# Performance work log

Measured on AMD Instinct MI355X. Metric: run time of the kernel, lower is better.

Reference implementation:

```python
import jax, jax.numpy as jnp
import numpy as np

# Fixed problem sizes (match input_specs): B graphs of N points each, kNN with K neighbors.
B, N, K = 32, 2048, 20
F_IN, H, C = 3, 64, 40
BN = B * N
E = BN * K


def mlp(x, w1, b1, w2, b2):
    # PyG MLP([in, H, H]) with plain last layer: Lin -> ReLU -> Lin
    return jax.nn.relu(x @ w1 + b1) @ w2 + b2


def edge_conv(x, src, dst, w1, b1, w2, b2):
    # EdgeConv message for edge j->i: MLP(cat[x_i, x_j - x_i]); aggr='max' at target i.
    xi = x[dst]                      # [E, F]
    xj = x[src]                      # [E, F]
    msg = mlp(jnp.concatenate([xi, xj - xi], axis=-1), w1, b1, w2, b2)  # [E, H]
    out = jax.ops.segment_max(msg, dst, num_segments=x.shape[0])        # [BN, H]
    # nodes with no incoming edges: -inf -> 0 (torch_scatter max fill behavior)
    return jnp.where(jnp.isfinite(out), out, jnp.zeros((), out.dtype))


def dynamic_edge_conv(x, w1, b1, w2, b2):
    # Rebuild kNN graph from current features within each graph, then EdgeConv(max).
    xb = x.reshape(B, N, -1)                                   # [B, N, H]
    sq = jnp.sum(xb * xb, axis=-1)                             # [B, N]
    # squared euclidean distances [B, N, N]
    d = sq[:, :, None] - 2.0 * jnp.einsum('bnh,bmh->bnm', xb, xb) + sq[:, None, :]
    _, idx = jax.lax.top_k(-d, K)                              # [B, N, K] nearest (incl. self)
    xj = jax.vmap(lambda xg, ig: xg[ig])(xb, idx)              # [B, N, K, H]
    xi = jnp.broadcast_to(xb[:, :, None, :], xj.shape)         # [B, N, K, H]
    msg = mlp(jnp.concatenate([xi, xj - xi], axis=-1), w1, b1, w2, b2)  # [B, N, K, H]
    return jnp.max(msg, axis=2).reshape(BN, -1)                # exactly K msgs per node


def _lin_init(key, fan_in, fan_out):
    k1, k2 = jax.random.split(key)
    s = 1.0 / np.sqrt(fan_in)
    w = jax.random.uniform(k1, (fan_in, fan_out), jnp.float32, -s, s)
    b = jax.random.uniform(k2, (fan_out,), jnp.float32, -s, s)
    return w, b


def setup_inputs() -> dict:
    key = jax.random.key(0)
    ks = jax.random.split(key, 10)
    x = jax.random.normal(ks[0], (BN, F_IN), jnp.float32)
    edge_index = jax.random.randint(ks[1], (2, E), 0, BN, jnp.int64)
    batch = (jnp.arange(BN) // N).astype(jnp.int64)
    c1_w1, c1_b1 = _lin_init(ks[2], 2 * F_IN, H)
    c1_w2, c1_b2 = _lin_init(ks[3], H, H)
    d1_w1, d1_b1 = _lin_init(ks[4], 2 * H, H)
    d1_w2, d1_b2 = _lin_init(ks[5], H, H)
    d2_w1, d2_b1 = _lin_init(ks[6], 2 * H, H)
    d2_w2, d2_b2 = _lin_init(ks[7], H, H)
    lin_w, lin_b = _lin_init(ks[8], H, C)
    return dict(x=x, edge_index=edge_index, batch=batch,
                c1_w1=c1_w1, c1_b1=c1_b1, c1_w2=c1_w2, c1_b2=c1_b2,
                d1_w1=d1_w1, d1_b1=d1_b1, d1_w2=d1_w2, d1_b2=d1_b2,
                d2_w1=d2_w1, d2_b1=d2_b1, d2_w2=d2_w2, d2_b2=d2_b2,
                lin_w=lin_w, lin_b=lin_b)


def reference(x, edge_index, batch,
              c1_w1, c1_b1, c1_w2, c1_b2,
              d1_w1, d1_b1, d1_w2, d1_b2,
              d2_w1, d2_b1, d2_w2, d2_b2,
              lin_w, lin_b):
    # batch is assumed sorted with equal-size graphs (arange // N); kNN is done per graph.
    src, dst = edge_index[0], edge_index[1]
    h = edge_conv(x, src, dst, c1_w1, c1_b1, c1_w2, c1_b2)
    h = dynamic_edge_conv(jax.nn.elu(h), d1_w1, d1_b1, d1_w2, d1_b2)
    h = dynamic_edge_conv(jax.nn.elu(h), d2_w1, d2_b1, d2_w2, d2_b2)
    return h @ lin_w + lin_b
```

## Files before the change

### kernel.cpp

```cpp
#include <hip/hip_runtime.h>
#include <math.h>

#define Bg 32
#define Ng 2048
#define Kn 20
#define BNn (Bg*Ng)
#define En (BNn*Kn)
#define Hd 64
#define Cd 40

#define KK 24
#define CAPB 7

typedef __attribute__((ext_vector_type(8))) short bf16x8;
typedef __attribute__((ext_vector_type(4))) float f32x4;

__device__ __forceinline__ unsigned enc_f32(float f){
  unsigned u = __float_as_uint(f);
  return ((int)u < 0) ? ~u : (u | 0x80000000u);
}

__device__ __forceinline__ unsigned short bf16rne(float f){
  unsigned u = __float_as_uint(f);
  return (unsigned short)((u + 0x7FFFu + ((u >> 16) & 1u)) >> 16);
}

__global__ void prep_w_kernel(const float* __restrict__ w1c, const float* __restrict__ w1d1,
                              const float* __restrict__ w1d2,
                              float* __restrict__ wpq0, float* __restrict__ wpq1,
                              float* __restrict__ wpq2){
  int t = blockIdx.x*256 + threadIdx.x;
  if (t < 3*128){
    int d = t >> 7, l = t & 127;
    wpq0[t] = (l < 64) ? (w1c[d*64 + l] - w1c[(d+3)*64 + l]) : w1c[(d+3)*64 + (l-64)];
  }
  if (t < 64*128){
    int d = t >> 7, l = t & 127;
    wpq1[t] = (l < 64) ? (w1d1[d*64 + l] - w1d1[(d+64)*64 + l]) : w1d1[(d+64)*64 + (l-64)];
    wpq2[t] = (l < 64) ? (w1d2[d*64 + l] - w1d2[(d+64)*64 + l]) : w1d2[(d+64)*64 + (l-64)];
  }
}

__global__ void zero_kernel(int* __restrict__ p){
  p[blockIdx.x*256 + threadIdx.x] = 0;
}

__global__ void init_enc_kernel(unsigned int* __restrict__ enc){
  enc[blockIdx.x*256 + threadIdx.x] = 0x007FFFFFu;
}

template<int D>
__global__ __launch_bounds__(128) void gemm_pq_kernel(const float* __restrict__ x,
                               const float* __restrict__ w,
                               float* __restrict__ P, float* __restrict__ Q){
  __shared__ float xs[8*D];
  int l = threadIdx.x;
  int node0 = blockIdx.x*8;
  float wc[D];
  #pragma unroll
  for (int d=0; d<D; d++) wc[d] = w[d*128 + l];
  for (int i=l; i < 8*D; i += 128) xs[i] = x[(size_t)node0*D + i];
  __syncthreads();
  #pragma unroll
  for (int n=0; n<8; n++){
    float s = 0.f;
    #pragma unroll
    for (int d=0; d<D; d++) s = fmaf(xs[n*D+d], wc[d], s);
    int node = node0 + n;
    if (l < 64) P[(size_t)node*64 + l] = s;
    else        Q[(size_t)node*64 + (l-64)] = s;
  }
}

__global__ __launch_bounds__(256) void sqxb_kernel(const float* __restrict__ x,
        float* __restrict__ sq, unsigned short* __restrict__ xb){
  int t = blockIdx.x*256 + threadIdx.x;
  int node = t >> 6, l = t & 63;
  float v = x[t];
  xb[t] = bf16rne(v);
  float s = v*v;
  #pragma unroll
  for (int o=32; o; o>>=1) s += __shfl_xor(s, o, 64);
  if (l == 0) sq[node] = s;
}

__global__ __launch_bounds__(256) void decode_sqxb_kernel(const unsigned int* __restrict__ enc,
        const float* __restrict__ b2, float* __restrict__ x,
        float* __restrict__ sq, unsigned short* __restrict__ xb){
  int t = blockIdx.x*256 + threadIdx.x;
  int node = t >> 6, l = t & 63;
  unsigned int e = enc[t];
  unsigned int bits = (e & 0x80000000u) ? (e ^ 0x80000000u) : ~e;
  float f = __uint_as_float(bits);
  if (isfinite(f)) f += b2[l]; else f = 0.f;
  f = f > 0.f ? f : expm1f(f);
  x[t] = f;
  xb[t] = bf16rne(f);
  float s = f*f;
  #pragma unroll
  for (int o=32; o; o>>=1) s += __shfl_xor(s, o, 64);
  if (l == 0) sq[node] = s;
}

__global__ void count_kernel(const int* __restrict__ ei, int* __restrict__ deg){
  int e = blockIdx.x*256 + threadIdx.x;
  atomicAdd(&deg[ei[En + e]], 1);
}

__global__ __launch_bounds__(1024) void scan_kernel(const int* __restrict__ deg,
        int* __restrict__ rowptr, int* __restrict__ cursor){
  __shared__ int ps[1024];
  int t = threadIdx.x;
  int base = t*64;
  int s = 0;
  for (int k=0;k<64;k++) s += deg[base+k];
  ps[t] = s; __syncthreads();
  for (int off=1; off<1024; off<<=1){
    int v = (t>=off) ? ps[t-off] : 0;
    __syncthreads();
    ps[t] += v;
    __syncthreads();
  }
  int run = (t>0) ? ps[t-1] : 0;
  for (int k=0;k<64;k++){
    rowptr[base+k] = run; cursor[base+k] = run;
    run += deg[base+k];
  }
  if (t==1023) rowptr[BNn] = run;
}

__global__ void scatter_kernel(const int* __restrict__ ei, int* __restrict__ cursor,
                               int* __restrict__ csrc, int* __restrict__ enid){
  int e = blockIdx.x*256 + threadIdx.x;
  int s = ei[e], d = ei[En + e];
  int pos = atomicAdd(&cursor[d], 1);
  csrc[pos] = s;
  enid[pos] = d;
}

#define FMA8(av, r) \
  acc[r][0]=fmaf(av,b0.x,acc[r][0]); acc[r][1]=fmaf(av,b0.y,acc[r][1]); \
  acc[r][2]=fmaf(av,b0.z,acc[r][2]); acc[r][3]=fmaf(av,b0.w,acc[r][3]); \
  acc[r][4]=fmaf(av,b1v.x,acc[r][4]); acc[r][5]=fmaf(av,b1v.y,acc[r][5]); \
  acc[r][6]=fmaf(av,b1v.z,acc[r][6]); acc[r][7]=fmaf(av,b1v.w,acc[r][7]);

__global__ __launch_bounds__(256,3) void econv_gemm_kernel(
    const int* __restrict__ csrc, const int* __restrict__ enid,
    const float* __restrict__ P, const float* __restrict__ Q,
    const float* __restrict__ b1, const float* __restrict__ w2,
    unsigned int* __restrict__ enc){
  __shared__ __align__(16) float As[32*256];
  __shared__ __align__(16) float Ws[64*64];
  __shared__ int eids[256];
  int tid = threadIdx.x;
  int e0 = ((blockIdx.x & 7)*640 + (blockIdx.x >> 3))*256;
  int e = e0 + tid;
  int j = csrc[e];
  int i = enid[e];
  eids[tid] = i;
  const float* Pr = P + (size_t)i*Hd;
  const float* Qr = Q + (size_t)j*Hd;
  #pragma unroll
  for (int c=0;c<16;c++) Ws[c*256 + tid] = w2[c*256 + tid];

  int m0 = tid >> 3, n0 = tid & 7;
  float acc[8][8];
  #pragma unroll
  for (int a=0;a<8;a++)
    #pragma unroll
    for (int b=0;b<8;b++) acc[a][b]=0.f;

  #pragma unroll 1
  for (int kh=0; kh<2; kh++){
    __syncthreads();
    #pragma unroll
    for (int c=0;c<8;c++){
      int k = kh*32 + 4*c;
      float4 q4 = *(const float4*)(Qr + k);
      float4 pk = *(const float4*)(Pr + k);
      float4 b4 = *(const float4*)(b1 + k);
      As[(4*c+0)*256 + tid] = fmaxf(pk.x+q4.x+b4.x, 0.f);
      As[(4*c+1)*256 + tid] = fmaxf(pk.y+q4.y+b4.y, 0.f);
      As[(4*c+2)*256 + tid] = fmaxf(pk.z+q4.z+b4.z, 0.f);
      As[(4*c+3)*256 + tid] = fmaxf(pk.w+q4.w+b4.w, 0.f);
    }
    __syncthreads();
    #pragma unroll 4
    for (int kk=0; kk<32; kk++){
      int k = kh*32 + kk;
      float4 a0 = *(const float4*)&As[kk*256 + 8*m0];
      float4 a1 = *(const float4*)&As[kk*256 + 8*m0 + 4];
      float4 b0 = *(const float4*)&Ws[k*64 + 8*n0];
      float4 b1v = *(const float4*)&Ws[k*64 + 8*n0 + 4];
      FMA8(a0.x, 0) FMA8(a0.y, 1) FMA8(a0.z, 2) FMA8(a0.w, 3)
      FMA8(a1.x, 4) FMA8(a1.y, 5) FMA8(a1.z, 6) FMA8(a1.w, 7)
    }
  }
  unsigned* lmax = (unsigned*)As;
  int nfirst = eids[0];
  __syncthreads();
  for (int z = tid; z < 32*65; z += 256) lmax[z] = 0u;
  __syncthreads();
  {
    int rbase = 8*m0;
    int cur = eids[rbase];
    float vmax[8];
    #pragma unroll
    for (int b=0;b<8;b++) vmax[b] = -INFINITY;
    #pragma unroll
    for (int a=0;a<8;a++){
      int id = eids[rbase + a];
      if (id != cur){
        int lid = cur - nfirst;
        if (lid < 32){
          #pragma unroll
          for (int b=0;b<8;b++) atomicMax(&lmax[lid*65 + 8*n0 + b], enc_f32(vmax[b]));
        } else {
          #pragma unroll
          for (int b=0;b<8;b++) atomicMax(&enc[(size_t)cur*Hd + 8*n0 + b], enc_f32(vmax[b]));
        }
        #pragma unroll
        for (int b=0;b<8;b++) vmax[b] = -INFINITY;
        cur = id;
      }
      #pragma unroll
      for (int b=0;b<8;b++) vmax[b] = fmaxf(vmax[b], acc[a][b]);
    }
    int lid = cur - nfirst;
    if (lid < 32){
      #pragma unroll
      for (int b=0;b<8;b++) atomicMax(&lmax[lid*65 + 8*n0 + b], enc_f32(vmax[b]));
    } else {
      #pragma unroll
      for (int b=0;b<8;b++) atomicMax(&enc[(size_t)cur*Hd + 8*n0 + b], enc_f32(vmax[b]));
    }
  }
  __syncthreads();
  {
    int ch = tid & 63;
    for (int lid = tid >> 6; lid < 32; lid += 4){
      unsigned v = lmax[lid*65 + ch];
      if (v) atomicMax(&enc[(size_t)(nfirst + lid)*Hd + ch], v);
    }
  }
}

__device__ __forceinline__ void ins24(unsigned (&kb)[KK], unsigned key){
  #pragma unroll
  for (int p=KK-1; p>0; p--){
    unsigned ins = (key < kb[p]) ? key : kb[p];
    kb[p] = (key < kb[p-1]) ? kb[p-1] : ins;
  }
  kb[0] = (key < kb[0]) ? key : kb[0];
}

#define KNN_FLUSH() do { \
  _Pragma("unroll 1") \
  for (int c=0;c<CAPB;c++){ \
    if (!__any(c < cnt)) break; \
    unsigned kf = (c < cnt) ? kc[c][tid] : 0xFFFFFFFFu; \
    ins24(kb, kf); \
  } \
  cnt = 0; kbLast = kb[KK-1]; \
} while(0)

#define KNN_TRY(key) do { unsigned kk_ = (key); \
  if (kk_ < kbLast){ kc[cnt][tid] = kk_; cnt++; } } while(0)

#define SWZ16(base, row, stridep2, byteoff) \
  ((unsigned short*)((char*)(base) + ((((row) << (stridep2)) + (byteoff)) ^ (((row) & 7) << 4))))

__global__ __launch_bounds__(256,4) void knn_kernel(
    const unsigned short* __restrict__ xb, const float* __restrict__ sq,
    unsigned short* __restrict__ cand){
  __shared__ __align__(16) unsigned short xjb[128*64];
  __shared__ __align__(16) unsigned short Dt[64*128];
  __shared__ unsigned kc[CAPB][256];
  __shared__ float sqs[128];

  int tid = threadIdx.x;
  int lane = tid & 63, w = tid >> 6;
  int bid = ((blockIdx.x & 7) << 7) | (blockIdx.x >> 3);
  int g  = bid >> 5;
  int r0 = (bid & 31) * 64;
  const unsigned short* xbg = xb + (size_t)g*Ng*Hd;
  const float* sg = sq + (size_t)g*Ng;

  int q = w;
  int prow = lane;
  int rw = w*16;

  bf16x8 A0, A1;
  {
    int arow = r0 + rw + (lane & 15);
    A0 = *(const bf16x8*)(xbg + (size_t)arow*Hd +      (lane>>4)*8);
    A1 = *(const bf16x8*)(xbg + (size_t)arow*Hd + 32 + (lane>>4)*8);
  }
  {
    int jr = tid >> 1, half = tid & 1;
    int jloc = (jr >> 5)*512 + (jr & 31);
    const uint4* src = (const uint4*)(xbg + (size_t)jloc*Hd + half*32);
    uint4 a = src[0], b = src[1], c2 = src[2], d2 = src[3];
    *(uint4*)SWZ16(xjb, jr, 7, half*64 +  0) = a;
    *(uint4*)SWZ16(xjb, jr, 7, half*64 + 16) = b;
    *(uint4*)SWZ16(xjb, jr, 7, half*64 + 32) = c2;
    *(uint4*)SWZ16(xjb, jr, 7, half*64 + 48) = d2;
    if (tid < 128) sqs[tid] = sg[(tid>>5)*512 + (tid&31)];
  }

  unsigned kb[KK];
  #pragma unroll
  for (int t=0;t<KK;t++) kb[t] = 0xFFFFFFFFu;
  unsigned kbLast = 0xFFFFFFFFu;
  int cnt = 0;

  __syncthreads();

  #pragma unroll 1
  for (int it = 0; it < 16; it++){
    uint4 pf0, pf1, pf2, pf3; float psq = 0.f;
    int itn = it + 1;
    int jr = tid >> 1, half = tid & 1;
    if (itn < 16){
      int jloc = (jr >> 5)*512 + itn*32 + (jr & 31);
      const uint4* src = (const uint4*)(xbg + (size_t)jloc*Hd + half*32);
      pf0 = src[0]; pf1 = src[1]; pf2 = src[2]; pf3 = src[3];
      if (tid < 128) psq = sg[(tid>>5)*512 + itn*32 + (tid&31)];
    }
    #pragma unroll
    for (int jb = 0; jb < 8; jb++){
      int brow = jb*16 + (lane & 15);
      bf16x8 B0 = *(const bf16x8*)SWZ16(xjb, brow, 7,      (lane>>4)*16);
      bf16x8 B1 = *(const bf16x8*)SWZ16(xjb, brow, 7, 64 + (lane>>4)*16);
      f32x4 acc = {0.f, 0.f, 0.f, 0.f};
      acc = __builtin_amdgcn_mfma_f32_16x16x32_bf16(A0, B0, acc, 0, 0, 0);
      acc = __builtin_amdgcn_mfma_f32_16x16x32_bf16(A1, B1, acc, 0, 0, 0);
      int col = jb*16 + (lane & 15);
      float sqv = sqs[col];
      int rbase = rw + (lane>>4)*4;
      #pragma unroll
      for (int v=0; v<4; v++){
        float f = fmaf(acc[v], -2.f, sqv);
        unsigned u = __float_as_uint(f);
        unsigned t2 = ((unsigned)((int)u >> 31)) | 0x8000u;
        *SWZ16(Dt, rbase + v, 8, col*2) = (unsigned short)((u >> 16) ^ t2);
      }
    }
    __syncthreads();
    if (it == 0){
      unsigned key[32];
      const char* dbase = (const char*)Dt + (prow << 8);
      unsigned m = (prow & 7) << 4;
      #pragma unroll
      for (int r4=0; r4<4; r4++){
        uint4 dv = *(const uint4*)(dbase + ((unsigned)(q*64 + r4*16) ^ m));
        int cb = q*512 + r4*8;
        key[r4*8+0] = (dv.x << 16) + (unsigned)(cb + 0);
        key[r4*8+1] = (dv.x & 0xFFFF0000u) | (unsigned)(cb + 1);
        key[r4*8+2] = (dv.y << 16) + (unsigned)(cb + 2);
        key[r4*8+3] = (dv.y & 0xFFFF0000u) | (unsigned)(cb + 3);
        key[r4*8+4] = (dv.z << 16) + (unsigned)(cb + 4);
        key[r4*8+5] = (dv.z & 0xFFFF0000u) | (unsigned)(cb + 5);
        key[r4*8+6] = (dv.w << 16) + (unsigned)(cb + 6);
        key[r4*8+7] = (dv.w & 0xFFFF0000u) | (unsigned)(cb + 7);
      }
      #pragma unroll
      for (int k2 = 2; k2 <= 32; k2 <<= 1){
        #pragma unroll
        for (int j2 = k2>>1; j2 > 0; j2 >>= 1){
          #pragma unroll
          for (int i2 = 0; i2 < 32; i2++){
            int ixj = i2 ^ j2;
            if (ixj > i2){
              unsigned a = key[i2], b = key[ixj];
              unsigned lo = a < b ? a : b;
              unsigned hi = a < b ? b : a;
              bool up = ((i2 & k2) == 0);
              key[i2]  = up ? lo : hi;
              key[ixj] = up ? hi : lo;
            }
          }
        }
      }
      #pragma unroll
      for (int t=0;t<KK;t++) kb[t] = key[t];
      kbLast = kb[KK-1];
    } else {
      int jbase0 = q*512 + it*32;
      const char* dbase = (const char*)Dt + (prow << 8);
      unsigned m = (prow & 7) << 4;
      #pragma unroll
      for (int r4=0; r4<4; r4++){
        uint4 dv = *(const uint4*)(dbase + ((unsigned)(q*64 + r4*16) ^ m));
        int cb = jbase0 + r4*8;
        KNN_TRY((dv.x << 16) + (unsigned)(cb + 0));
        KNN_TRY((dv.x & 0xFFFF0000u) | (unsigned)(cb + 1));
        KNN_TRY((dv.y << 16) + (unsigned)(cb + 2));
        KNN_TRY((dv.y & 0xFFFF0000u) | (unsigned)(cb + 3));
        if (__any(cnt >= 4)) KNN_FLUSH();
        KNN_TRY((dv.z << 16) + (unsigned)(cb + 4));
        KNN_TRY((dv.z & 0xFFFF0000u) | (unsigned)(cb + 5));
        KNN_TRY((dv.w << 16) + (unsigned)(cb + 6));
        KNN_TRY((dv.w & 0xFFFF0000u) | (unsigned)(cb + 7));
        if (__any(cnt >= 4)) KNN_FLUSH();
      }
    }
    if (itn < 16){
      *(uint4*)SWZ16(xjb, jr, 7, half*64 +  0) = pf0;
      *(uint4*)SWZ16(xjb, jr, 7, half*64 + 16) = pf1;
      *(uint4*)SWZ16(xjb, jr, 7, half*64 + 32) = pf2;
      *(uint4*)SWZ16(xjb, jr, 7, half*64 + 48) = pf3;
      if (tid < 128) sqs[tid] = psq;
    }
    __syncthreads();
  }
  KNN_FLUSH();
  size_t base = (size_t)(g*Ng + r0 + prow)*96 + q*24;
  #pragma unroll
  for (int t=0;t<KK;t++)
    cand[base + t] = (unsigned short)(kb[t] & 2047u);
}

__global__ __launch_bounds__(256,2) void rerank_kernel(const float* __restrict__ x,
        const unsigned short* __restrict__ cand, int* __restrict__ idx){
  __shared__ __align__(16) unsigned long long ks[4][96];
  int tid = threadIdx.x;
  int lane = tid & 63, w = tid >> 6;
  int bid = ((blockIdx.x & 7) << 11) | (blockIdx.x >> 3);
  int row = bid*4 + w;
  int g = row >> 11;
  const float* xg = x + (size_t)g*Ng*Hd;
  int chunk = lane & 3;
  int cg = lane >> 2;
  const float* xr = x + (size_t)row*Hd;
  float4 xc[4];
  #pragma unroll
  for (int it2=0; it2<4; it2++) xc[it2] = *(const float4*)(xr + 16*it2 + 4*chunk);

  int js[6];
  #pragma unroll
  for (int p=0; p<6; p++) js[p] = cand[(size_t)row*96 + p*16 + cg];

  float4 bb[6][4];
  #pragma unroll
  for (int p=0; p<6; p++){
    const float* xj = xg + (size_t)js[p]*Hd;
    #pragma unroll
    for (int it2=0; it2<4; it2++) bb[p][it2] = *(const float4*)(xj + 16*it2 + 4*chunk);
  }
  #pragma unroll
  for (int p=0; p<6; p++){
    float dot = 0.f, sqj = 0.f;
    #pragma unroll
    for (int it2=0; it2<4; it2++){
      float4 b = bb[p][it2];
      float4 a = xc[it2];
      dot = fmaf(a.x, b.x, dot); dot = fmaf(a.y, b.y, dot);
      dot = fmaf(a.z, b.z, dot); dot = fmaf(a.w, b.w, dot);
      sqj = fmaf(b.x, b.x, sqj); sqj = fmaf(b.y, b.y, sqj);
      sqj = fmaf(b.z, b.z, sqj); sqj = fmaf(b.w, b.w, sqj);
    }
    dot += __shfl_xor(dot, 1, 64); dot += __shfl_xor(dot, 2, 64);
    sqj += __shfl_xor(sqj, 1, 64); sqj += __shfl_xor(sqj, 2, 64);
    if (chunk == 0){
      float dist = fmaf(dot, -2.f, sqj);
      ks[w][p*16 + cg] = ((unsigned long long)enc_f32(dist) << 32) | (unsigned)js[p];
    }
  }
  __syncthreads();
  unsigned long long k0 = ks[w][lane];
  unsigned long long k1 = (lane < 32) ? ks[w][64 + lane] : ~0ULL;
  int r0 = 0, r1 = 0;
  #pragma unroll
  for (int c=0;c<96;c+=2){
    unsigned long long a = ks[w][c], b = ks[w][c+1];
    r0 += (a < k0) + (b < k0);
    r1 += (a < k1) + (b < k1);
  }
  if (r0 < Kn) idx[(size_t)row*Kn + r0] = g*Ng + (int)(k0 & 2047ULL);
  if (lane < 32 && r1 < Kn) idx[(size_t)row*Kn + r1] = g*Ng + (int)(k1 & 2047ULL);
}

__global__ __launch_bounds__(256,3) void emsg_kernel(
    const int* __restrict__ srcl,
    const float* __restrict__ P, const float* __restrict__ Q,
    const float* __restrict__ b1, const float* __restrict__ w2,
    unsigned int* __restrict__ enc){
  __shared__ __align__(16) char smem[49152];
  unsigned short* Ah = (unsigned short*)smem;
  unsigned short* Al = (unsigned short*)(smem + 16384);
  unsigned short* Wh = (unsigned short*)(smem + 32768);
  unsigned short* Wl = (unsigned short*)(smem + 40960);
  float* p0 = (float*)smem;
  float* p1 = (float*)(smem + 8448);
  int tid = threadIdx.x;
  int lane = tid & 63, w = tid >> 6;
  int e0 = ((blockIdx.x & 7)*640 + (blockIdx.x >> 3))*256;

  #pragma unroll
  for (int z = 0; z < 16; z++){
    int idx = z*256 + tid;
    int k = idx >> 6, n = idx & 63;
    float f = w2[idx];
    unsigned short h = bf16rne(f);
    float fh = __uint_as_float((unsigned)h << 16);
    unsigned short l = bf16rne(f - fh);
    *SWZ16(Wh, n, 7, k*2) = h;
    *SWZ16(Wl, n, 7, k*2) = l;
  }

  #pragma unroll 1
  for (int hh = 0; hh < 2; hh++){
    int eh0 = e0 + hh*128;
    __syncthreads();
    {
      int el = tid >> 1, kh = (tid & 1) * 32;
      int e = eh0 + el;
      int i = e / Kn;
      int j = srcl[e];
      const float* Pr = P + (size_t)i*Hd + kh;
      const float* Qr = Q + (size_t)j*Hd + kh;
      const float* Br = b1 + kh;
      #pragma unroll
      for (int m = 0; m < 4; m++){
        float4 pa = ((const float4*)Pr)[2*m], pb = ((const float4*)Pr)[2*m+1];
        float4 qa = ((const float4*)Qr)[2*m], qb = ((const float4*)Qr)[2*m+1];
        float4 ba = ((const float4*)Br)[2*m], bbv = ((const float4*)Br)[2*m+1];
        float a[8];
        a[0]=fmaxf(pa.x+qa.x+ba.x,0.f);  a[1]=fmaxf(pa.y+qa.y+ba.y,0.f);
        a[2]=fmaxf(pa.z+qa.z+ba.z,0.f);  a[3]=fmaxf(pa.w+qa.w+ba.w,0.f);
        a[4]=fmaxf(pb.x+qb.x+bbv.x,0.f); a[5]=fmaxf(pb.y+qb.y+bbv.y,0.f);
        a[6]=fmaxf(pb.z+qb.z+bbv.z,0.f); a[7]=fmaxf(pb.w+qb.w+bbv.w,0.f);
        unsigned hw[4], lw[4];
        #pragma unroll
        for (int t=0;t<4;t++){
          unsigned short h0 = bf16rne(a[2*t]);
          unsigned short h1 = bf16rne(a[2*t+1]);
          float f0 = __uint_as_float((unsigned)h0 << 16);
          float f1 = __uint_as_float((unsigned)h1 << 16);
          unsigned short l0 = bf16rne(a[2*t] - f0);
          unsigned short l1 = bf16rne(a[2*t+1] - f1);
          hw[t] = (unsigned)h0 | ((unsigned)h1 << 16);
          lw[t] = (unsigned)l0 | ((unsigned)l1 << 16);
        }
        uint4 hv = {hw[0], hw[1], hw[2], hw[3]};
        uint4 lv = {lw[0], lw[1], lw[2], lw[3]};
        *(uint4*)SWZ16(Ah, el, 7, (kh + 8*m)*2) = hv;
        *(uint4*)SWZ16(Al, el, 7, (kh + 8*m)*2) = lv;
      }
    }
    __syncthreads();
    bf16x8 Af[2][2], Lf[2][2];
    #pragma unroll
    for (int mt=0; mt<2; mt++)
      #pragma unroll
      for (int s=0; s<2; s++){
        int row = w*32 + mt*16 + (lane & 15);
        Af[mt][s] = *(const bf16x8*)SWZ16(Ah, row, 7, (s*32 + (lane>>4)*8)*2);
        Lf[mt][s] = *(const bf16x8*)SWZ16(Al, row, 7, (s*32 + (lane>>4)*8)*2);
      }
    f32x4 acc[2][4];
    #pragma unroll
    for (int mt=0; mt<2; mt++)
      #pragma unroll
      for (int nt=0; nt<4; nt++)
        acc[mt][nt] = (f32x4){0.f,0.f,0.f,0.f};
    #pragma unroll
    for (int nt=0; nt<4; nt++){
      int n = nt*16 + (lane & 15);
      bf16x8 Bh0 = *(const bf16x8*)SWZ16(Wh, n, 7, ((lane>>4)*8)*2);
      bf16x8 Bh1 = *(const bf16x8*)SWZ16(Wh, n, 7, (32 + (lane>>4)*8)*2);
      bf16x8 Bl0 = *(const bf16x8*)SWZ16(Wl, n, 7, ((lane>>4)*8)*2);
      bf16x8 Bl1 = *(const bf16x8*)SWZ16(Wl, n, 7, (32 + (lane>>4)*8)*2);
      #pragma unroll
      for (int mt=0; mt<2; mt++){
        f32x4 a_ = acc[mt][nt];
        a_ = __builtin_amdgcn_mfma_f32_16x16x32_bf16(Af[mt][0], Bh0, a_, 0, 0, 0);
        a_ = __builtin_amdgcn_mfma_f32_16x16x32_bf16(Af[mt][1], Bh1, a_, 0, 0, 0);
        a_ = __builtin_amdgcn_mfma_f32_16x16x32_bf16(Af[mt][0], Bl0, a_, 0, 0, 0);
        a_ = __builtin_amdgcn_mfma_f32_16x16x32_bf16(Af[mt][1], Bl1, a_, 0, 0, 0);
        a_ = __builtin_amdgcn_mfma_f32_16x16x32_bf16(Lf[mt][0], Bh0, a_, 0, 0, 0);
        a_ = __builtin_amdgcn_mfma_f32_16x16x32_bf16(Lf[mt][1], Bh1, a_, 0, 0, 0);
        acc[mt][nt] = a_;
      }
    }
    __syncthreads();
    #pragma unroll
    for (int mt=0; mt<2; mt++){
      int rb = w*32 + mt*16 + (lane>>4)*4;
      int rbg = eh0 + rb;
      int nd0 = rbg / Kn;
      int split = (nd0+1)*Kn - rbg; if (split > 4) split = 4;
      int cm = rb >> 2;
      #pragma unroll
      for (int nt=0; nt<4; nt++){
        int ch = nt*16 + (lane & 15);
        float s0v = -INFINITY, s1v = -INFINITY;
        #pragma unroll
        for (int v=0; v<4; v++){
          float val = acc[mt][nt][v];
          if (v < split) s0v = fmaxf(s0v, val); else s1v = fmaxf(s1v, val);
        }
        p0[ch*33 + cm] = s0v;
        p1[ch*33 + cm] = s1v;
      }
    }
    __syncthreads();
    int nfirst = eh0 / Kn;
    int ncnt = (eh0 + 127) / Kn - nfirst + 1;
    int ch = tid & 63;
    for (int ln = tid >> 6; ln < ncnt; ln += 4){
      int nd = nfirst + ln;
      int glo = nd*Kn;      if (glo < eh0)     glo = eh0;
      int ghi = nd*Kn + Kn; if (ghi > eh0+128) ghi = eh0+128;
      int mlo = (glo - eh0) >> 2, mhi = (ghi - 1 - eh0) >> 2;
      float v = -INFINITY;
      for (int mm = mlo; mm <= mhi; mm++){
        int bn = (eh0 + 4*mm) / Kn;
        if (bn == nd)     v = fmaxf(v, p0[ch*33 + mm]);
        if (bn + 1 == nd) v = fmaxf(v, p1[ch*33 + mm]);
      }
      atomicMax(&enc[(size_t)nd*Hd + ch], enc_f32(v));
    }
  }
}

__global__ __launch_bounds__(256) void decode_kernel(const unsigned int* __restrict__ enc,
         const float* __restrict__ b2, float* __restrict__ x){
  int t = blockIdx.x*256 + threadIdx.x;
  unsigned int e = enc[t];
  unsigned int bits = (e & 0x80000000u) ? (e ^ 0x80000000u) : ~e;
  float f = __uint_as_float(bits);
  if (isfinite(f)) f += b2[t & 63]; else f = 0.f;
  x[t] = f;
}

__global__ __launch_bounds__(64) void final_kernel(const float* __restrict__ h,
        const float* __restrict__ w, const float* __restrict__ bias,
        float* __restrict__ out){
  __shared__ float xs[Hd];
  int c = threadIdx.x;
  float wc[Hd];
  float bc = 0.f;
  if (c < Cd){
    #pragma unroll
    for (int d=0; d<Hd; d++) wc[d] = w[d*Cd + c];
    bc = bias[c];
  }
  for (int i = blockIdx.x; i < BNn; i += gridDim.x){
    __syncthreads();
    xs[c] = h[(size_t)i*Hd + c];
    __syncthreads();
    if (c < Cd){
      float s = bc;
      #pragma unroll
      for (int d=0; d<Hd; d++) s = fmaf(xs[d], wc[d], s);
      out[(size_t)i*Cd + c] = s;
    }
  }
}

extern "C" void kernel_launch(void* const* d_in, const int* in_sizes, int n_in,
                              void* d_out, int out_size, void* d_ws, size_t ws_size,
                              hipStream_t stream){
  const float* x0   = (const float*)d_in[0];
  const int*   ei   = (const int*)d_in[1];
  const float* c1w1 = (const float*)d_in[3];
  const float* c1b1 = (const float*)d_in[4];
  const float* c1w2 = (const float*)d_in[5];
  const float* c1b2 = (const float*)d_in[6];
  const float* d1w1 = (const float*)d_in[7];
  const float* d1b1 = (const float*)d_in[8];
  const float* d1w2 = (const float*)d_in[9];
  const float* d1b2 = (const float*)d_in[10];
  const float* d2w1 = (const float*)d_in[11];
  const float* d2b1 = (const float*)d_in[12];
  const float* d2w2 = (const float*)d_in[13];
  const float* d2b2 = (const float*)d_in[14];
  const float* linw = (const float*)d_in[15];
  const float* linb = (const float*)d_in[16];
  float* out = (float*)d_out;

  char* ws = (char*)d_ws;
  size_t off = 0;
  auto alloc = [&](size_t bytes)->char*{
    char* p = ws + off; off += (bytes + 255) & ~(size_t)255; return p;
  };
  float*        X    = (float*)alloc(sizeof(float)*(size_t)BNn*Hd);
  float*        P    = (float*)alloc(sizeof(float)*(size_t)BNn*Hd);
  float*        Q    = (float*)alloc(sizeof(float)*(size_t)BNn*Hd);
  float*        H2   = (float*)alloc(sizeof(float)*(size_t)BNn*Hd);
  unsigned int* ENC  = (unsigned int*)alloc(sizeof(unsigned)*(size_t)BNn*Hd);
  int*          SHRD = (int*)alloc(sizeof(int)*(size_t)En);
  int*          DEG  = (int*)alloc(sizeof(int)*BNn);
  int*          RPTR = (int*)alloc(sizeof(int)*(BNn+1));
  int*          CUR  = (int*)alloc(sizeof(int)*BNn);
  float*        SQ   = (float*)alloc(sizeof(float)*BNn);
  float*        WPQ0 = (float*)alloc(sizeof(float)*3*128);
  float*        WPQ1 = (float*)alloc(sizeof(float)*64*128);
  float*        WPQ2 = (float*)alloc(sizeof(float)*64*128);
  int*            CSRC = SHRD;
  int*            IDX  = SHRD;
  int*            ENID = (int*)H2;
  unsigned short* XB   = (unsigned short*)H2;
  unsigned short* CAND = (unsigned short*)ENC;
  (void)ws_size; (void)in_sizes; (void)n_in; (void)out_size;

  prep_w_kernel<<<32, 256, 0, stream>>>(c1w1, d1w1, d2w1, WPQ0, WPQ1, WPQ2);
  zero_kernel<<<BNn/256, 256, 0, stream>>>(DEG);
  count_kernel<<<En/256, 256, 0, stream>>>(ei, DEG);
  gemm_pq_kernel<3><<<BNn/8, 128, 0, stream>>>(x0, WPQ0, P, Q);
  scan_kernel<<<1, 1024, 0, stream>>>(DEG, RPTR, CUR);
  scatter_kernel<<<En/256, 256, 0, stream>>>(ei, CUR, CSRC, ENID);
  init_enc_kernel<<<BNn*Hd/256, 256, 0, stream>>>(ENC);
  econv_gemm_kernel<<<En/256, 256, 0, stream>>>(CSRC, ENID, P, Q, c1b1, c1w2, ENC);
  decode_sqxb_kernel<<<BNn*Hd/256, 256, 0, stream>>>(ENC, c1b2, X, SQ, XB);

  gemm_pq_kernel<64><<<BNn/8, 128, 0, stream>>>(X, WPQ1, P, Q);
  knn_kernel<<<Bg*32, 256, 0, stream>>>(XB, SQ, CAND);
  rerank_kernel<<<BNn/4, 256, 0, stream>>>(X, CAND, IDX);
  init_enc_kernel<<<BNn*Hd/256, 256, 0, stream>>>(ENC);
  emsg_kernel<<<En/256, 256, 0, stream>>>(IDX, P, Q, d1b1, d1w2, ENC);
  decode_sqxb_kernel<<<BNn*Hd/256, 256, 0, stream>>>(ENC, d1b2, X, SQ, XB);

  gemm_pq_kernel<64><<<BNn/8, 128, 0, stream>>>(X, WPQ2, P, Q);
  knn_kernel<<<Bg*32, 256, 0, stream>>>(XB, SQ, CAND);
  rerank_kernel<<<BNn/4, 256, 0, stream>>>(X, CAND, IDX);
  init_enc_kernel<<<BNn*Hd/256, 256, 0, stream>>>(ENC);
  emsg_kernel<<<En/256, 256, 0, stream>>>(IDX, P, Q, d2b1, d2w2, ENC);
  decode_kernel<<<BNn*Hd/256, 256, 0, stream>>>(ENC, d2b2, H2);

  final_kernel<<<8192, 64, 0, stream>>>(H2, linw, linb, out);
}
```

Before: 1.337 ms.

## Use split-bf16 MFMA for first EdgeConv second-layer GEMM

Replaces the scalar FP32 FMA GEMM in the first EdgeConv kernel with bf16 MFMA instructions. Activations and weights are split into high and low bf16 parts, and three products are summed to keep near-FP32 accuracy. Edges are processed in two halves of 128. The max-aggregation now goes through a transposed, swizzled LDS tile, with per-column run-length atomicMax straight to global memory instead of an LDS pre-reduction stage. This moves compute onto the matrix cores but may raise global atomic traffic and adds split/convert overhead.

```diff
diff --git a/kernel.cpp b/kernel.cpp
--- a/kernel.cpp
+++ b/kernel.cpp
@@ -138,109 +138,143 @@
   enid[pos] = d;
 }
 
-#define FMA8(av, r) \
-  acc[r][0]=fmaf(av,b0.x,acc[r][0]); acc[r][1]=fmaf(av,b0.y,acc[r][1]); \
-  acc[r][2]=fmaf(av,b0.z,acc[r][2]); acc[r][3]=fmaf(av,b0.w,acc[r][3]); \
-  acc[r][4]=fmaf(av,b1v.x,acc[r][4]); acc[r][5]=fmaf(av,b1v.y,acc[r][5]); \
-  acc[r][6]=fmaf(av,b1v.z,acc[r][6]); acc[r][7]=fmaf(av,b1v.w,acc[r][7]);
+#define SWZ16(base, row, stridep2, byteoff) \
+  ((unsigned short*)((char*)(base) + ((((row) << (stridep2)) + (byteoff)) ^ (((row) & 7) << 4))))
 
 __global__ __launch_bounds__(256,3) void econv_gemm_kernel(
     const int* __restrict__ csrc, const int* __restrict__ enid,
     const float* __restrict__ P, const float* __restrict__ Q,
     const float* __restrict__ b1, const float* __restrict__ w2,
     unsigned int* __restrict__ enc){
-  __shared__ __align__(16) float As[32*256];
-  __shared__ __align__(16) float Ws[64*64];
+  __shared__ __align__(16) char smem[49152];
+  unsigned short* Ah = (unsigned short*)smem;
+  unsigned short* Al = (unsigned short*)(smem + 16384);
+  unsigned short* Wh = (unsigned short*)(smem + 32768);
+  unsigned short* Wl = (unsigned short*)(smem + 40960);
+  float* Ct = (float*)smem;
   __shared__ int eids[256];
   int tid = threadIdx.x;
+  int lane = tid & 63, w = tid >> 6;
   int e0 = ((blockIdx.x & 7)*640 + (blockIdx.x >> 3))*256;
-  int e = e0 + tid;
-  int j = csrc[e];
-  int i = enid[e];
-  eids[tid] = i;
-  const float* Pr = P + (size_t)i*Hd;
-  const float* Qr = Q + (size_t)j*Hd;
-  #pragma unroll
-  for (int c=0;c<16;c++) Ws[c*256 + tid] = w2[c*256 + tid];
-
-  int m0 = tid >> 3, n0 = tid & 7;
-  float acc[8][8];
-  #pragma unroll
-  for (int a=0;a<8;a++)
-    #pragma unroll
-    for (int b=0;b<8;b++) acc[a][b]=0.f;
+
+  eids[tid] = enid[e0 + tid];
+  #pragma unroll
+  for (int z = 0; z < 16; z++){
+    int idx = z*256 + tid;
+    int k = idx >> 6, n = idx & 63;
+    float f = w2[idx];
+    unsigned short h = bf16rne(f);
+    float fh = __uint_as_float((unsigned)h << 16);
+    unsigned short l = bf16rne(f - fh);
+    *SWZ16(Wh, n, 7, k*2) = h;
+    *SWZ16(Wl, n, 7, k*2) = l;
+  }
 
   #pragma unroll 1
-  for (int kh=0; kh<2; kh++){
-    __syncthreads();
-    #pragma unroll
-    for (int c=0;c<8;c++){
-      int k = kh*32 + 4*c;
-      float4 q4 = *(const float4*)(Qr + k);
-      float4 pk = *(const float4*)(Pr + k);
-      float4 b4 = *(const float4*)(b1 + k);
-      As[(4*c+0)*256 + tid] = fmaxf(pk.x+q4.x+b4.x, 0.f);
-      As[(4*c+1)*256 + tid] = fmaxf(pk.y+q4.y+b4.y, 0.f);
-      As[(4*c+2)*256 + tid] = fmaxf(pk.z+q4.z+b4.z, 0.f);
-      As[(4*c+3)*256 + tid] = fmaxf(pk.w+q4.w+b4.w, 0.f);
-    }
-    __syncthreads();
-    #pragma unroll 4
-    for (int kk=0; kk<32; kk++){
-      int k = kh*32 + kk;
-      float4 a0 = *(const float4*)&As[kk*256 + 8*m0];
-      float4 a1 = *(const float4*)&As[kk*256 + 8*m0 + 4];
-      float4 b0 = *(const float4*)&Ws[k*64 + 8*n0];
-      float4 b1v = *(const float4*)&Ws[k*64 + 8*n0 + 4];
-      FMA8(a0.x, 0) FMA8(a0.y, 1) FMA8(a0.z, 2) FMA8(a0.w, 3)
-      FMA8(a1.x, 4) FMA8(a1.y, 5) FMA8(a1.z, 6) FMA8(a1.w, 7)
-    }
-  }
-  unsigned* lmax = (unsigned*)As;
-  int nfirst = eids[0];
-  __syncthreads();
-  for (int z = tid; z < 32*65; z += 256) lmax[z] = 0u;
-  __syncthreads();
-  {
-    int rbase = 8*m0;
-    int cur = eids[rbase];
-    float vmax[8];
-    #pragma unroll
-    for (int b=0;b<8;b++) vmax[b] = -INFINITY;
-    #pragma unroll
-    for (int a=0;a<8;a++){
-      int id = eids[rbase + a];
-      if (id != cur){
-        int lid = cur - nfirst;
-        if (lid < 32){
-          #pragma unroll
-          for (int b=0;b<8;b++) atomicMax(&lmax[lid*65 + 8*n0 + b], enc_f32(vmax[b]));
-        } else {
-          #pragma unroll
-          for (int b=0;b<8;b++) atomicMax(&enc[(size_t)cur*Hd + 8*n0 + b], enc_f32(vmax[b]));
+  for (int hh = 0; hh < 2; hh++){
+    int eh0 = e0 + hh*128;
+    __syncthreads();
+    {
+      int el = tid >> 1, kh2 = (tid & 1) * 32;
+      int e = eh0 + el;
+      int i = eids[hh*128 + el];
+      int j = csrc[e];
+      const float* Pr = P + (size_t)i*Hd + kh2;
+      const float* Qr = Q + (size_t)j*Hd + kh2;
+      const float* Br = b1 + kh2;
+      #pragma unroll
+      for (int m = 0; m < 4; m++){
+        float4 pa = ((const float4*)Pr)[2*m], pb = ((const float4*)Pr)[2*m+1];
+        float4 qa = ((const float4*)Qr)[2*m], qb = ((const float4*)Qr)[2*m+1];
+        float4 ba = ((const float4*)Br)[2*m], bbv = ((const float4*)Br)[2*m+1];
+        float a[8];
+        a[0]=fmaxf(pa.x+qa.x+ba.x,0.f);  a[1]=fmaxf(pa.y+qa.y+ba.y,0.f);
+        a[2]=fmaxf(pa.z+qa.z+ba.z,0.f);  a[3]=fmaxf(pa.w+qa.w+ba.w,0.f);
+        a[4]=fmaxf(pb.x+qb.x+bbv.x,0.f); a[5]=fmaxf(pb.y+qb.y+bbv.y,0.f);
+        a[6]=fmaxf(pb.z+qb.z+bbv.z,0.f); a[7]=fmaxf(pb.w+qb.w+bbv.w,0.f);
+        unsigned hw[4], lw[4];
+        #pragma unroll
+        for (int t=0;t<4;t++){
+          unsigned short h0 = bf16rne(a[2*t]);
+          unsigned short h1 = bf16rne(a[2*t+1]);
+          float f0 = __uint_as_float((unsigned)h0 << 16);
+          float f1 = __uint_as_float((unsigned)h1 << 16);
+          unsigned short l0 = bf16rne(a[2*t] - f0);
+          unsigned short l1 = bf16rne(a[2*t+1] - f1);
+          hw[t] = (unsigned)h0 | ((unsigned)h1 << 16);
+          lw[t] = (unsigned)l0 | ((unsigned)l1 << 16);
         }
+        uint4 hv = {hw[0], hw[1], hw[2], hw[3]};
+        uint4 lv = {lw[0], lw[1], lw[2], lw[3]};
+        *(uint4*)SWZ16(Ah, el, 7, (kh2 + 8*m)*2) = hv;
+        *(uint4*)SWZ16(Al, el, 7, (kh2 + 8*m)*2) = lv;
+      }
+    }
+    __syncthreads();
+    bf16x8 Af[2][2], Lf[2][2];
+    #pragma unroll
+    for (int mt=0; mt<2; mt++)
+      #pragma unroll
+      for (int s=0; s<2; s++){
+        int row = w*32 + mt*16 + (lane & 15);
+        Af[mt][s] = *(const bf16x8*)SWZ16(Ah, row, 7, (s*32 + (lane>>4)*8)*2);
+        Lf[mt][s] = *(const bf16x8*)SWZ16(Al, row, 7, (s*32 + (lane>>4)*8)*2);
+      }
+    f32x4 acc[2][4];
+    #pragma unroll
+    for (int mt=0; mt<2; mt++)
+      #pragma unroll
+      for (int nt=0; nt<4; nt++)
+        acc[mt][nt] = (f32x4){0.f,0.f,0.f,0.f};
+    #pragma unroll
+    for (int nt=0; nt<4; nt++){
+      int n = nt*16 + (lane & 15);
+      bf16x8 Bh0 = *(const bf16x8*)SWZ16(Wh, n, 7, ((lane>>4)*8)*2);
+      bf16x8 Bh1 = *(const bf16x8*)SWZ16(Wh, n, 7, (32 + (lane>>4)*8)*2);
+      bf16x8 Bl0 = *(const bf16x8*)SWZ16(Wl, n, 7, ((lane>>4)*8)*2);
+      bf16x8 Bl1 = *(const bf16x8*)SWZ16(Wl, n, 7, (32 + (lane>>4)*8)*2);
+      #pragma unroll
+      for (int mt=0; mt<2; mt++){
+        f32x4 a_ = acc[mt][nt];
+        a_ = __builtin_amdgcn_mfma_f32_16x16x32_bf16(Af[mt][0], Bh0, a_, 0, 0, 0);
+        a_ = __builtin_amdgcn_mfma_f32_16x16x32_bf16(Af[mt][1], Bh1, a_, 0, 0, 0);
+        a_ = __builtin_amdgcn_mfma_f32_16x16x32_bf16(Af[mt][0], Bl0, a_, 0, 0, 0);
+        a_ = __builtin_amdgcn_mfma_f32_16x16x32_bf16(Af[mt][1], Bl1, a_, 0, 0, 0);
+        a_ = __builtin_amdgcn_mfma_f32_16x16x32_bf16(Lf[mt][0], Bh0, a_, 0, 0, 0);
+        a_ = __builtin_amdgcn_mfma_f32_16x16x32_bf16(Lf[mt][1], Bh1, a_, 0, 0, 0);
+        acc[mt][nt] = a_;
+      }
+    }
+    __syncthreads();
+    #pragma unroll
+    for (int mt=0; mt<2; mt++){
+      int rb = w*32 + mt*16 + (lane>>4)*4;
+      #pragma unroll
+      for (int nt=0; nt<4; nt++){
+        int ch = nt*16 + (lane & 15);
         #pragma unroll
-        for (int b=0;b<8;b++) vmax[b] = -INFINITY;
-        cur = id;
-      }
-      #pragma unroll
-      for (int b=0;b<8;b++) vmax[b] = fmaxf(vmax[b], acc[a][b]);
-    }
-    int lid = cur - nfirst;
-    if (lid < 32){
-      #pragma unroll
-      for (int b=0;b<8;b++) atomicMax(&lmax[lid*65 + 8*n0 + b], enc_f32(vmax[b]));
-    } else {
-      #pragma unroll
-      for (int b=0;b<8;b++) atomicMax(&enc[(size_t)cur*Hd + 8*n0 + b], enc_f32(vmax[b]));
-    }
-  }
-  __syncthreads();
-  {
-    int ch = tid & 63;
-    for (int lid = tid >> 6; lid < 32; lid += 4){
-      unsigned v = lmax[lid*65 + ch];
-      if (v) atomicMax(&enc[(size_t)(nfirst + lid)*Hd + ch], v);
+        for (int v=0; v<4; v++)
+          Ct[ch*128 + ((rb+v) ^ (ch & 31))] = acc[mt][nt][v];
+      }
+    }
+    __syncthreads();
+    {
+      int ch = tid & 63, part = tid >> 6;
+      int rbase = part*32;
+      int cur = eids[hh*128 + rbase];
+      float vmax = -INFINITY;
+      #pragma unroll 1
+      for (int r = 0; r < 32; r++){
+        int row = rbase + r;
+        int id = eids[hh*128 + row];
+        float v = Ct[ch*128 + (row ^ (ch & 31))];
+        if (id != cur){
+          atomicMax(&enc[(size_t)cur*Hd + ch], enc_f32(vmax));
+          vmax = -INFINITY; cur = id;
+        }
+        vmax = fmaxf(vmax, v);
+      }
+      atomicMax(&enc[(size_t)cur*Hd + ch], enc_f32(vmax));
     }
   }
 }
@@ -266,9 +300,6 @@
 
 #define KNN_TRY(key) do { unsigned kk_ = (key); \
   if (kk_ < kbLast){ kc[cnt][tid] = kk_; cnt++; } } while(0)
-
-#define SWZ16(base, row, stridep2, byteoff) \
-  ((unsigned short*)((char*)(base) + ((((row) << (stridep2)) + (byteoff)) ^ (((row) & 7) << 4))))
 
 __global__ __launch_bounds__(256,4) void knn_kernel(
     const unsigned short* __restrict__ xb, const float* __restrict__ sq,
```

After: 1.333 ms. Within noise of the previous version (-0.3%).
